# Performance work log

Hardware: AMD Instinct MI355X
Metric: run time of the kernel (lower is better)

The kernel has to match this reference:

```python
import jax, jax.numpy as jnp
import numpy as np

H = 768
NH = 12
HD = 64
R = 4
SCALING = 8.0 / 4.0  # lora_alpha / r


def setup_inputs() -> dict:
    key = jax.random.key(0)
    ks = jax.random.split(key, 16)
    B, T = 16, 512
    s = 0.02
    x = jax.random.normal(ks[0], (B, T, H), dtype=jnp.float32)
    mask = jax.random.randint(ks[1], (B, T), 0, 2, dtype=jnp.int32)
    return {
        "x": x,
        "mask": mask,
        "Wq": jax.random.normal(ks[2], (H, H), jnp.float32) * s,
        "bq": jnp.zeros((H,), jnp.float32),
        "Aq": jax.random.normal(ks[3], (R, H), jnp.float32) * s,
        "Bq": jax.random.normal(ks[4], (H, R), jnp.float32) * s,
        "Wk": jax.random.normal(ks[5], (H, H), jnp.float32) * s,
        "bk": jnp.zeros((H,), jnp.float32),
        "Wv": jax.random.normal(ks[6], (H, H), jnp.float32) * s,
        "bv": jnp.zeros((H,), jnp.float32),
        "Av": jax.random.normal(ks[7], (R, H), jnp.float32) * s,
        "Bv": jax.random.normal(ks[8], (H, R), jnp.float32) * s,
        "Wo": jax.random.normal(ks[9], (H, H), jnp.float32) * s,
        "bo": jnp.zeros((H,), jnp.float32),
    }


def _lora_linear(x, W, b, A, Bm):
    # base: x @ W^T + b ; lora: (x @ A^T) @ B^T * scaling (dropout inactive at eval)
    return x @ W.T + b + (x @ A.T) @ Bm.T * SCALING


def reference(x, mask, Wq, bq, Aq, Bq, Wk, bk, Wv, bv, Av, Bv, Wo, bo):
    B, T, _ = x.shape
    q = _lora_linear(x, Wq, bq, Aq, Bq).reshape(B, T, NH, HD).transpose(0, 2, 1, 3)
    k = (x @ Wk.T + bk).reshape(B, T, NH, HD).transpose(0, 2, 1, 3)
    v = _lora_linear(x, Wv, bv, Av, Bv).reshape(B, T, NH, HD).transpose(0, 2, 1, 3)
    # [B, NH, T, T]
    scores = jnp.einsum("bhqd,bhkd->bhqk", q, k) / jnp.sqrt(jnp.float32(HD))
    m = (mask == 0)[:, None, None, :]  # mask key positions where mask==0
    scores = jnp.where(m, jnp.float32(-1e9), scores)
    attn = jax.nn.softmax(scores, axis=-1)  # dropout inactive at eval
    out = jnp.einsum("bhqk,bhkd->bhqd", attn, v)
    out = out.transpose(0, 2, 1, 3).reshape(B, T, H)
    return out @ Wo.T + bo
```

## Files before the change

kernel.cpp:

```cpp
#include <hip/hip_runtime.h>
#include <stdint.h>

#define H 768
#define NHEAD 12
#define HDIM 64
#define BATCH 16
#define TSEQ 512
#define BT (BATCH*TSEQ)
#define C3 (3*H)
#define LDQK 1536

typedef __attribute__((ext_vector_type(8))) short short8;
typedef __attribute__((ext_vector_type(4))) float floatx4;
typedef unsigned short u16;

__device__ __forceinline__ u16 f2bf(float f) {
    union { float f; unsigned int u; } v; v.f = f;
    unsigned int u = v.u;
    return (u16)((u + 0x7FFFu + ((u >> 16) & 1u)) >> 16);
}

__device__ __forceinline__ void async_ld16(const void* g, void* l) {
    __builtin_amdgcn_global_load_lds((__attribute__((address_space(1))) void*)g,
                                     (__attribute__((address_space(3))) void*)l,
                                     16, 0, 0);
}

__global__ void prep_weights(const float* __restrict__ Wq, const float* __restrict__ bq,
                             const float* __restrict__ Aq, const float* __restrict__ Bq,
                             const float* __restrict__ Wk, const float* __restrict__ bk,
                             const float* __restrict__ Wv, const float* __restrict__ bv,
                             const float* __restrict__ Av, const float* __restrict__ Bv,
                             const float* __restrict__ Wo,
                             u16* __restrict__ Wall, u16* __restrict__ Wobf,
                             float* __restrict__ bias_all)
{
    const int idx = blockIdx.x * 256 + threadIdx.x;
    const int r = idx / H;
    const int c = idx - r * H;
    if (r < H) {
        float v = Wq[idx] + 2.0f * (Bq[r*4+0]*Aq[c] + Bq[r*4+1]*Aq[H+c] +
                                    Bq[r*4+2]*Aq[2*H+c] + Bq[r*4+3]*Aq[3*H+c]);
        Wall[idx] = f2bf(v);
    } else if (r < 2*H) {
        Wall[idx] = f2bf(Wk[idx - H*H]);
    } else if (r < 3*H) {
        const int rr = r - 2*H;
        float v = Wv[rr*H + c] + 2.0f * (Bv[rr*4+0]*Av[c] + Bv[rr*4+1]*Av[H+c] +
                                         Bv[rr*4+2]*Av[2*H+c] + Bv[rr*4+3]*Av[3*H+c]);
        Wall[idx] = f2bf(v);
    } else {
        Wobf[idx - 3*H*H] = f2bf(Wo[idx - 3*H*H]);
    }
    if (idx < C3) {
        bias_all[idx] = (idx < H) ? bq[idx] : (idx < 2*H ? bk[idx - H] : bv[idx - 2*H]);
    }
}

__global__ void cvt_x_kernel(const float* __restrict__ x, u16* __restrict__ xb)
{
    const int i = (blockIdx.x * 256 + threadIdx.x) * 4;
    const float4 v = *(const float4*)(x + i);
    u16 o[4] = { f2bf(v.x), f2bf(v.y), f2bf(v.z), f2bf(v.w) };
    *(uint2*)(xb + i) = *(const uint2*)o;
}

template<int MODE, int TM>
__global__ __launch_bounds__(256)
void gemm_bt(const u16* __restrict__ A, const u16* __restrict__ Bw,
             const float* __restrict__ bias, void* __restrict__ Cout,
             u16* __restrict__ Vout, int K, int ldc)
{
    constexpr int MT = TM / 32;
    __shared__ u16 Ablk[2][TM * 32];
    __shared__ u16 Bblk[2][128 * 32];
    const int tid  = threadIdx.x;
    const int wave = tid >> 6;
    const int lane = tid & 63;
    const int quad = lane >> 4;
    const int l16  = lane & 15;
    const int m0 = blockIdx.y * TM;
    const int n0 = blockIdx.x * 128;
    const int mw = (wave & 1) * (TM / 2);
    const int nw = (wave >> 1) * 64;

    const int srow = lane >> 2;
    const int scol = (lane & 3) * 8;
    const int arow0 = wave * (TM / 4);
    const u16* gA = A  + (size_t)(m0 + arow0 + srow) * K + scol;
    const u16* gB = Bw + (size_t)(n0 + wave*32 + srow) * K + scol;

    floatx4 acc[MT][4] = {};

    auto stage = [&](int k0, int pp) {
        u16* lA = Ablk[pp] + arow0 * 32;
        u16* lB = Bblk[pp] + wave * 32 * 32;
        async_ld16(gA + k0, lA);
        if (TM == 128) async_ld16(gA + k0 + 16*K, lA + 16*32);
        async_ld16(gB + k0, lB);
        async_ld16(gB + k0 + 16*K, lB + 16*32);
    };

    auto compute = [&](int pp) {
        short8 af[MT], bfr[4];
        #pragma unroll
        for (int mt = 0; mt < MT; mt++)
            af[mt] = *(const short8*)(Ablk[pp] + (mw + mt*16 + l16)*32 + quad*8);
        #pragma unroll
        for (int nt = 0; nt < 4; nt++)
            bfr[nt] = *(const short8*)(Bblk[pp] + (nw + nt*16 + l16)*32 + quad*8);
        #pragma unroll
        for (int mt = 0; mt < MT; mt++)
            #pragma unroll
            for (int nt = 0; nt < 4; nt++)
                acc[mt][nt] = __builtin_amdgcn_mfma_f32_16x16x32_bf16(af[mt], bfr[nt], acc[mt][nt], 0, 0, 0);
    };

    const int nIter = K >> 5;
    stage(0, 0);
    for (int it = 0; it < nIter; it++) {
        __syncthreads();
        if (it + 1 < nIter) stage((it + 1) * 32, (it + 1) & 1);
        compute(it & 1);
    }

    if (MODE == 1 && n0 >= LDQK) {
        const int nv = n0 + nw - LDQK;
        const int b  = m0 >> 9;
        #pragma unroll
        for (int nt = 0; nt < 4; nt++) {
            const int n  = nv + nt*16 + l16;
            const int hh = n >> 6, d = n & 63;
            const float bv = bias[LDQK + n];
            u16* vp = Vout + ((size_t)(b*NHEAD + hh) * HDIM + d) * TSEQ;
            #pragma unroll
            for (int mt = 0; mt < MT; mt++) {
                const int t0 = (m0 & 511) + mw + mt*16 + quad*4;
                u16 pack[4];
                #pragma unroll
                for (int r = 0; r < 4; r++) pack[r] = f2bf(acc[mt][nt][r] + bv);
                *(uint2*)(vp + t0) = *(const uint2*)pack;
            }
        }
    } else {
        #pragma unroll
        for (int nt = 0; nt < 4; nt++) {
            const int n = n0 + nw + nt*16 + l16;
            const float bv = bias[n];
            #pragma unroll
            for (int mt = 0; mt < MT; mt++) {
                #pragma unroll
                for (int r = 0; r < 4; r++) {
                    const int m = m0 + mw + mt*16 + quad*4 + r;
                    const float v = acc[mt][nt][r] + bv;
                    if (MODE == 1) ((u16*)Cout)[(size_t)m * ldc + n] = f2bf(v);
                    else           ((float*)Cout)[(size_t)m * ldc + n] = v;
                }
            }
        }
    }
}

#define PSTRIDE 40

__global__ __launch_bounds__(256)
void attn_kernel(const u16* __restrict__ qk, const u16* __restrict__ vt,
                 const int* __restrict__ mask, u16* __restrict__ attn_out)
{
    __shared__ float maskadd[TSEQ];
    __shared__ u16 Kbuf[2][32 * 64];
    __shared__ u16 Vbuf[2][64 * 32];
    __shared__ u16 Pbuf[4][2][16 * PSTRIDE];

    const int qt = blockIdx.x;
    const int bh = blockIdx.y;
    const int b = bh / NHEAD, h = bh - b * NHEAD;
    const int tid  = threadIdx.x;
    const int wave = tid >> 6;
    const int lane = tid & 63;
    const int quad = lane >> 4;
    const int l16  = lane & 15;

    for (int i = tid; i < TSEQ; i += 256)
        maskadd[i] = (mask[b*TSEQ + i] == 0) ? -1e9f : 0.0f;

    const size_t btok = (size_t)b * TSEQ;
    const int q0 = qt * 128 + wave * 32;

    short8 qf[2][2];
    #pragma unroll
    for (int m = 0; m < 2; m++) {
        const u16* qp = qk + (btok + q0 + m*16 + l16) * LDQK + h*HDIM + quad*8;
        qf[m][0] = *(const short8*)qp;
        qf[m][1] = *(const short8*)(qp + 32);
    }

    const u16* kglob = qk + btok * LDQK + H + h*HDIM;
    const u16* vglob = vt + (size_t)bh * HDIM * TSEQ;

    auto stage = [&](int kb, int pp) {
        {
            const int r = lane >> 3;
            const int g = (lane & 7) ^ r;
            async_ld16(kglob + (size_t)(kb + wave*8 + r) * LDQK + g*8,
                       &Kbuf[pp][wave*8*64]);
        }
        {
            const int dr = lane >> 2;
            const int g  = (lane & 3) ^ ((dr >> 1) & 3);
            async_ld16(vglob + (size_t)(wave*16 + dr) * TSEQ + kb + g*8,
                       &Vbuf[pp][wave*16*32]);
        }
    };

    floatx4 o[2][4] = {};
    float lsum[2][4] = {};

    auto compute = [&](int kb, int pp) {
        const u16* Kb_ = Kbuf[pp];
        const u16* Vb_ = Vbuf[pp];
        short8 kf[2][2];
        #pragma unroll
        for (int t = 0; t < 2; t++)
            #pragma unroll
            for (int h2 = 0; h2 < 2; h2++)
                kf[t][h2] = *(const short8*)(Kb_ + (t*16 + l16)*64 + (((h2*4 + quad) ^ (l16 & 7))*8));
        short8 vf[4];
        #pragma unroll
        for (int dt = 0; dt < 4; dt++)
            vf[dt] = *(const short8*)(Vb_ + (dt*16 + l16)*32 + ((quad ^ ((l16 >> 1) & 3))*8));

        floatx4 s[2][2];
        #pragma unroll
        for (int m = 0; m < 2; m++)
            #pragma unroll
            for (int t = 0; t < 2; t++) {
                floatx4 acc = {0.f, 0.f, 0.f, 0.f};
                acc = __builtin_amdgcn_mfma_f32_16x16x32_bf16(qf[m][0], kf[t][0], acc, 0, 0, 0);
                acc = __builtin_amdgcn_mfma_f32_16x16x32_bf16(qf[m][1], kf[t][1], acc, 0, 0, 0);
                s[m][t] = acc;
            }
        const float m0 = maskadd[kb + l16];
        const float m1 = maskadd[kb + 16 + l16];
        #pragma unroll
        for (int m = 0; m < 2; m++) {
            u16* Pw = Pbuf[wave][m];
            #pragma unroll
            for (int r = 0; r < 4; r++) {
                const float p0 = __expf(s[m][0][r] * 0.125f + m0);
                const float p1 = __expf(s[m][1][r] * 0.125f + m1);
                lsum[m][r] += p0 + p1;
                Pw[(quad*4 + r) * PSTRIDE + l16]      = f2bf(p0);
                Pw[(quad*4 + r) * PSTRIDE + 16 + l16] = f2bf(p1);
            }
        }
        #pragma unroll
        for (int m = 0; m < 2; m++) {
            const short8 pa = *(const short8*)(Pbuf[wave][m] + l16 * PSTRIDE + quad*8);
            #pragma unroll
            for (int dt = 0; dt < 4; dt++)
                o[m][dt] = __builtin_amdgcn_mfma_f32_16x16x32_bf16(pa, vf[dt], o[m][dt], 0, 0, 0);
        }
    };

    stage(0, 0);
    for (int it = 0; it < 16; it++) {
        __syncthreads();
        if (it < 15) stage((it + 1) * 32, (it + 1) & 1);
        compute(it * 32, it & 1);
    }

    #pragma unroll
    for (int m = 0; m < 2; m++) {
        float inv[4];
        #pragma unroll
        for (int r = 0; r < 4; r++) {
            float l = lsum[m][r];
            l += __shfl_xor(l, 1);
            l += __shfl_xor(l, 2);
            l += __shfl_xor(l, 4);
            l += __shfl_xor(l, 8);
            inv[r] = 1.0f / l;
        }
        #pragma unroll
        for (int dt = 0; dt < 4; dt++)
            #pragma unroll
            for (int r = 0; r < 4; r++) {
                const int q = q0 + m*16 + quad*4 + r;
                attn_out[(btok + q) * H + h*HDIM + dt*16 + l16] = f2bf(o[m][dt][r] * inv[r]);
            }
    }
}

extern "C" void kernel_launch(void* const* d_in, const int* in_sizes, int n_in,
                              void* d_out, int out_size, void* d_ws, size_t ws_size,
                              hipStream_t stream)
{
    const float* x   = (const float*)d_in[0];
    const int* mask  = (const int*)d_in[1];
    const float* Wq  = (const float*)d_in[2];
    const float* bq  = (const float*)d_in[3];
    const float* Aq  = (const float*)d_in[4];
    const float* Bq  = (const float*)d_in[5];
    const float* Wk  = (const float*)d_in[6];
    const float* bk  = (const float*)d_in[7];
    const float* Wv  = (const float*)d_in[8];
    const float* bv  = (const float*)d_in[9];
    const float* Av  = (const float*)d_in[10];
    const float* Bv  = (const float*)d_in[11];
    const float* Wo  = (const float*)d_in[12];
    const float* bo  = (const float*)d_in[13];

    char* ws = (char*)d_ws;
    u16*   xb      = (u16*)  (ws);
    u16*   Wall    = (u16*)  (ws + 12582912);
    u16*   Wobf    = (u16*)  (ws + 16121856);
    float* biasall = (float*)(ws + 17301504);
    u16*   qk      = (u16*)  (ws + 17310720);
    u16*   vt      = (u16*)  (ws + 42476544);
    u16*   attn_o  = (u16*)  (ws + 55059456);

    prep_weights<<<(4*H*H)/256, 256, 0, stream>>>(Wq, bq, Aq, Bq, Wk, bk, Wv, bv,
                                                  Av, Bv, Wo, Wall, Wobf, biasall);
    cvt_x_kernel<<<(BT*H)/1024, 256, 0, stream>>>(x, xb);
    gemm_bt<1,128><<<dim3(C3/128, BT/128), 256, 0, stream>>>(xb, Wall, biasall, qk, vt, H, LDQK);
    attn_kernel<<<dim3(TSEQ/128, BATCH*NHEAD), 256, 0, stream>>>(qk, vt, mask, attn_o);
    gemm_bt<0,64><<<dim3(H/128, BT/64), 256, 0, stream>>>(attn_o, Wobf, bo, d_out, nullptr, H, H);
}
```

Baseline: 221.3 us.

## Merge weight prep and x conversion into one launch; single-buffer GEMM LDS

The weight-preparation and x-to-bf16 conversion kernels are combined into one launch that dispatches on block index, removing one kernel launch and its gap. The GEMM drops its double-buffered LDS prefetch in favour of a single buffer with load, sync, compute per k-step. This halves LDS use and may raise occupancy, but global-load latency is no longer overlapped with MFMA work inside a block.

```diff
diff --git a/kernel.cpp b/kernel.cpp
--- a/kernel.cpp
+++ b/kernel.cpp
@@ -26,16 +26,26 @@
                                      16, 0, 0);
 }
 
-__global__ void prep_weights(const float* __restrict__ Wq, const float* __restrict__ bq,
-                             const float* __restrict__ Aq, const float* __restrict__ Bq,
-                             const float* __restrict__ Wk, const float* __restrict__ bk,
-                             const float* __restrict__ Wv, const float* __restrict__ bv,
-                             const float* __restrict__ Av, const float* __restrict__ Bv,
-                             const float* __restrict__ Wo,
-                             u16* __restrict__ Wall, u16* __restrict__ Wobf,
-                             float* __restrict__ bias_all)
+#define PREP_BLOCKS 9216
+#define CVT_BLOCKS  6144
+__global__ void prep_kernel(const float* __restrict__ Wq, const float* __restrict__ bq,
+                            const float* __restrict__ Aq, const float* __restrict__ Bq,
+                            const float* __restrict__ Wk, const float* __restrict__ bk,
+                            const float* __restrict__ Wv, const float* __restrict__ bv,
+                            const float* __restrict__ Av, const float* __restrict__ Bv,
+                            const float* __restrict__ Wo, const float* __restrict__ x,
+                            u16* __restrict__ Wall, u16* __restrict__ Wobf,
+                            float* __restrict__ bias_all, u16* __restrict__ xb)
 {
-    const int idx = blockIdx.x * 256 + threadIdx.x;
+    const int bid = blockIdx.x;
+    if (bid >= PREP_BLOCKS) {
+        const int i = ((bid - PREP_BLOCKS) * 256 + threadIdx.x) * 4;
+        const float4 v = *(const float4*)(x + i);
+        u16 o[4] = { f2bf(v.x), f2bf(v.y), f2bf(v.z), f2bf(v.w) };
+        *(uint2*)(xb + i) = *(const uint2*)o;
+        return;
+    }
+    const int idx = bid * 256 + threadIdx.x;
     const int r = idx / H;
     const int c = idx - r * H;
     if (r < H) {
@@ -57,14 +67,6 @@
     }
 }
 
-__global__ void cvt_x_kernel(const float* __restrict__ x, u16* __restrict__ xb)
-{
-    const int i = (blockIdx.x * 256 + threadIdx.x) * 4;
-    const float4 v = *(const float4*)(x + i);
-    u16 o[4] = { f2bf(v.x), f2bf(v.y), f2bf(v.z), f2bf(v.w) };
-    *(uint2*)(xb + i) = *(const uint2*)o;
-}
-
 template<int MODE, int TM>
 __global__ __launch_bounds__(256)
 void gemm_bt(const u16* __restrict__ A, const u16* __restrict__ Bw,
@@ -72,8 +74,8 @@
              u16* __restrict__ Vout, int K, int ldc)
 {
     constexpr int MT = TM / 32;
-    __shared__ u16 Ablk[2][TM * 32];
-    __shared__ u16 Bblk[2][128 * 32];
+    __shared__ u16 Ablk[TM * 32];
+    __shared__ u16 Bblk[128 * 32];
     const int tid  = threadIdx.x;
     const int wave = tid >> 6;
     const int lane = tid & 63;
@@ -89,39 +91,30 @@
     const int arow0 = wave * (TM / 4);
     const u16* gA = A  + (size_t)(m0 + arow0 + srow) * K + scol;
     const u16* gB = Bw + (size_t)(n0 + wave*32 + srow) * K + scol;
+    u16* lA = Ablk + arow0 * 32;
+    u16* lB = Bblk + wave * 32 * 32;
 
     floatx4 acc[MT][4] = {};
 
-    auto stage = [&](int k0, int pp) {
-        u16* lA = Ablk[pp] + arow0 * 32;
-        u16* lB = Bblk[pp] + wave * 32 * 32;
+    for (int k0 = 0; k0 < K; k0 += 32) {
+        __syncthreads();
         async_ld16(gA + k0, lA);
         if (TM == 128) async_ld16(gA + k0 + 16*K, lA + 16*32);
         async_ld16(gB + k0, lB);
         async_ld16(gB + k0 + 16*K, lB + 16*32);
-    };
-
-    auto compute = [&](int pp) {
+        __syncthreads();
         short8 af[MT], bfr[4];
         #pragma unroll
         for (int mt = 0; mt < MT; mt++)
-            af[mt] = *(const short8*)(Ablk[pp] + (mw + mt*16 + l16)*32 + quad*8);
+            af[mt] = *(const short8*)(Ablk + (mw + mt*16 + l16)*32 + quad*8);
         #pragma unroll
         for (int nt = 0; nt < 4; nt++)
-            bfr[nt] = *(const short8*)(Bblk[pp] + (nw + nt*16 + l16)*32 + quad*8);
+            bfr[nt] = *(const short8*)(Bblk + (nw + nt*16 + l16)*32 + quad*8);
         #pragma unroll
         for (int mt = 0; mt < MT; mt++)
             #pragma unroll
             for (int nt = 0; nt < 4; nt++)
                 acc[mt][nt] = __builtin_amdgcn_mfma_f32_16x16x32_bf16(af[mt], bfr[nt], acc[mt][nt], 0, 0, 0);
-    };
-
-    const int nIter = K >> 5;
-    stage(0, 0);
-    for (int it = 0; it < nIter; it++) {
-        __syncthreads();
-        if (it + 1 < nIter) stage((it + 1) * 32, (it + 1) & 1);
-        compute(it & 1);
     }
 
     if (MODE == 1 && n0 >= LDQK) {
@@ -320,9 +313,8 @@
     u16*   vt      = (u16*)  (ws + 42476544);
     u16*   attn_o  = (u16*)  (ws + 55059456);
 
-    prep_weights<<<(4*H*H)/256, 256, 0, stream>>>(Wq, bq, Aq, Bq, Wk, bk, Wv, bv,
-                                                  Av, Bv, Wo, Wall, Wobf, biasall);
-    cvt_x_kernel<<<(BT*H)/1024, 256, 0, stream>>>(x, xb);
+    prep_kernel<<<PREP_BLOCKS + CVT_BLOCKS, 256, 0, stream>>>(
+        Wq, bq, Aq, Bq, Wk, bk, Wv, bv, Av, Bv, Wo, x, Wall, Wobf, biasall, xb);
     gemm_bt<1,128><<<dim3(C3/128, BT/128), 256, 0, stream>>>(xb, Wall, biasall, qk, vt, H, LDQK);
     attn_kernel<<<dim3(TSEQ/128, BATCH*NHEAD), 256, 0, stream>>>(qk, vt, mask, attn_o);
     gemm_bt<0,64><<<dim3(H/128, BT/64), 256, 0, stream>>>(attn_o, Wobf, bo, d_out, nullptr, H, H);
```

Result: no change. 223.6 us (+1.0%).
